# Kernel optimization log

Measured on AMD Instinct MI355X. Metric: run time of the kernel, lower is better.

Reference implementation:

```python
import jax, jax.numpy as jnp
import numpy as np

N = 100_000      # points
F = 64           # feature dim
B = 4            # graphs in batch
POOL_RAD = 0.2   # voxel size
D = 8            # static upper bound on voxels per spatial dim
M_MAX = 1024     # static upper bound on number of nonempty clusters


def setup_inputs() -> dict:
    key = jax.random.key(0)
    k1, k2, k3 = jax.random.split(key, 3)
    pos = jax.random.uniform(k1, (N, 3), dtype=jnp.float32)
    x = jax.random.normal(k2, (N, F), dtype=jnp.float32)
    batch = jnp.sort(jax.random.randint(k3, (N,), 0, B)).astype(jnp.int32)
    return {"pos": pos, "x": x, "batch": batch}


def reference(pos, x, batch):
    batch = batch.astype(jnp.int32)
    rad = jnp.asarray(POOL_RAD, pos.dtype)
    # --- voxel_grid clustering (start = min - rad/2 as in the torch module) ---
    start = pos.min(axis=0) - rad * 0.5
    coords = jnp.clip(jnp.floor((pos - start) / rad).astype(jnp.int32), 0, D - 1)  # [N,3]
    vox = ((batch * D + coords[:, 0]) * D + coords[:, 1]) * D + coords[:, 2]       # [N]
    V = B * D * D * D
    # --- consecutive_cluster + scatter mean of positions ---
    ones = jnp.ones((pos.shape[0],), pos.dtype)
    counts = jax.ops.segment_sum(ones, vox, num_segments=V)       # [V]
    sum_pos = jax.ops.segment_sum(pos, vox, num_segments=V)       # [V,3]
    nonempty = counts > 0
    # compact nonempty voxels to static M_MAX slots (padding duplicates voxel idx 0;
    # argmin tie-breaking to the first index keeps duplicates inert)
    idx = jnp.nonzero(nonempty, size=M_MAX, fill_value=0)[0]      # [M_MAX]
    valid = jnp.arange(M_MAX) < jnp.sum(nonempty)                 # [M_MAX]
    centroids = sum_pos[idx] / jnp.maximum(counts[idx], 1.0)[:, None]  # [M_MAX,3]
    new_batch = idx // (D * D * D)                                # [M_MAX]
    # --- nearest: assign each point to nearest cluster centroid in same graph ---
    d2 = (jnp.sum(pos * pos, axis=1)[:, None]
          - 2.0 * pos @ centroids.T
          + jnp.sum(centroids * centroids, axis=1)[None, :])      # [N, M_MAX]
    big = jnp.asarray(1e30, pos.dtype)
    d2 = jnp.where((batch[:, None] == new_batch[None, :]) & valid[None, :], d2, big)
    assign = jnp.argmin(d2, axis=1)                               # [N]
    # --- scatter max of features into clusters (empty clusters -> 0, as in PyG) ---
    x_pool = jax.ops.segment_max(x, assign, num_segments=M_MAX)   # [M_MAX, F]
    x_pool = jnp.where(jnp.isfinite(x_pool), x_pool, jnp.zeros_like(x_pool))
    return x_pool, centroids, new_batch, valid
```

## Files before the change

### kernel.cpp

```cpp
#include <hip/hip_runtime.h>
#include <stdint.h>

#define DGRID 8
#define NVOX  2048
#define NBATCH 4
#define MMAX  1024
#define FDIM  64
#define WIN   1024

__device__ __forceinline__ unsigned encf(float f){
  unsigned u = __float_as_uint(f);
  return (u & 0x80000000u) ? ~u : (u | 0x80000000u);
}
__device__ __forceinline__ float decf(unsigned e){
  unsigned u = (e & 0x80000000u) ? (e ^ 0x80000000u) : ~e;
  return __uint_as_float(u);
}


__global__ __launch_bounds__(256) void k_minpart(const float* __restrict__ pos,
    int N, unsigned* __restrict__ bmin, int* __restrict__ counts,
    int* __restrict__ clustCnt){
  if (blockIdx.x < 8) counts[blockIdx.x * 256 + threadIdx.x] = 0;
  else if (blockIdx.x < 12) clustCnt[(blockIdx.x - 8) * 256 + threadIdx.x] = 0;
  unsigned m0 = 0xFFFFFFFFu, m1 = 0xFFFFFFFFu, m2 = 0xFFFFFFFFu;
  int stride = gridDim.x * blockDim.x;
  for (int i = blockIdx.x * blockDim.x + threadIdx.x; i < N; i += stride){
    unsigned e0 = encf(pos[3*i+0]); if (e0 < m0) m0 = e0;
    unsigned e1 = encf(pos[3*i+1]); if (e1 < m1) m1 = e1;
    unsigned e2 = encf(pos[3*i+2]); if (e2 < m2) m2 = e2;
  }
  #pragma unroll
  for (int off = 32; off > 0; off >>= 1){
    unsigned t0 = __shfl_down(m0, off); if (t0 < m0) m0 = t0;
    unsigned t1 = __shfl_down(m1, off); if (t1 < m1) m1 = t1;
    unsigned t2 = __shfl_down(m2, off); if (t2 < m2) m2 = t2;
  }
  __shared__ unsigned sm[4][3];
  int wv = threadIdx.x >> 6, lane = threadIdx.x & 63;
  if (lane == 0){ sm[wv][0] = m0; sm[wv][1] = m1; sm[wv][2] = m2; }
  __syncthreads();
  if (threadIdx.x == 0){
    unsigned a0 = sm[0][0], a1 = sm[0][1], a2 = sm[0][2];
    for (int k = 1; k < 4; k++){
      if (sm[k][0] < a0) a0 = sm[k][0];
      if (sm[k][1] < a1) a1 = sm[k][1];
      if (sm[k][2] < a2) a2 = sm[k][2];
    }
    bmin[blockIdx.x*3+0] = a0;
    bmin[blockIdx.x*3+1] = a1;
    bmin[blockIdx.x*3+2] = a2;
  }
}

__global__ __launch_bounds__(256) void k_voxcnt(const float* __restrict__ pos,
    const int* __restrict__ batch, int N, const unsigned* __restrict__ bmin,
    int* __restrict__ vox, int* __restrict__ counts){
  __shared__ unsigned smin[3];
  if (threadIdx.x < 64){
    unsigned a0 = bmin[threadIdx.x*3+0];
    unsigned a1 = bmin[threadIdx.x*3+1];
    unsigned a2 = bmin[threadIdx.x*3+2];
    #pragma unroll
    for (int off = 32; off > 0; off >>= 1){
      unsigned t0 = __shfl_down(a0, off); if (t0 < a0) a0 = t0;
      unsigned t1 = __shfl_down(a1, off); if (t1 < a1) a1 = t1;
      unsigned t2 = __shfl_down(a2, off); if (t2 < a2) a2 = t2;
    }
    if (threadIdx.x == 0){ smin[0] = a0; smin[1] = a1; smin[2] = a2; }
  }
  __syncthreads();
  int i = blockIdx.x * 256 + threadIdx.x;
  if (i >= N) return;
  float s0 = __fsub_rn(decf(smin[0]), 0.1f);
  float s1 = __fsub_rn(decf(smin[1]), 0.1f);
  float s2 = __fsub_rn(decf(smin[2]), 0.1f);
  float q0 = __fdiv_rn(__fsub_rn(pos[3*i+0], s0), 0.2f);
  float q1 = __fdiv_rn(__fsub_rn(pos[3*i+1], s1), 0.2f);
  float q2 = __fdiv_rn(__fsub_rn(pos[3*i+2], s2), 0.2f);
  int c0 = (int)floorf(q0); c0 = c0 < 0 ? 0 : (c0 > DGRID-1 ? DGRID-1 : c0);
  int c1 = (int)floorf(q1); c1 = c1 < 0 ? 0 : (c1 > DGRID-1 ? DGRID-1 : c1);
  int c2 = (int)floorf(q2); c2 = c2 < 0 ? 0 : (c2 > DGRID-1 ? DGRID-1 : c2);
  int v = ((batch[i]*DGRID + c0)*DGRID + c1)*DGRID + c2;
  vox[i] = v;
  atomicAdd(&counts[v], 1);
}

__global__ __launch_bounds__(64) void k_scan_fast(const int* __restrict__ counts,
    int* Mout, int* batchStartC, int* batchPtr, int* __restrict__ idxOfCluster){
  int lane = threadIdx.x;
  int cs[32];
  int ne = 0, tot = 0;
  #pragma unroll
  for (int j = 0; j < 32; j++){
    int c = counts[lane*32 + j];
    cs[j] = c;
    ne += (c > 0) ? 1 : 0;
    tot += c;
  }
  int inc = ne, incT = tot;
  #pragma unroll
  for (int off = 1; off < 64; off <<= 1){
    int t  = __shfl_up(inc,  off);
    int tt = __shfl_up(incT, off);
    if (lane >= off){ inc += t; incT += tt; }
  }
  int exne = inc - ne;
  int exT  = incT - tot;
  int run = exne;
  #pragma unroll
  for (int j = 0; j < 32; j++){
    if (cs[j] > 0){
      if (run < MMAX) idxOfCluster[run] = lane*32 + j;
      run++;
    }
  }
  int M = __shfl(run, 63);
  for (int m = M + lane; m < MMAX; m += 64) idxOfCluster[m] = 0;
  int ex0  = __shfl(exne, 0),  ex16 = __shfl(exne, 16);
  int ex32 = __shfl(exne, 32), ex48 = __shfl(exne, 48);
  int t0 = __shfl(exT, 0),  t16 = __shfl(exT, 16);
  int t32 = __shfl(exT, 32), t48 = __shfl(exT, 48);
  int tN = __shfl(incT, 63);
  if (lane == 0){
    Mout[0] = M;
    batchStartC[0] = ex0;  batchStartC[1] = ex16;
    batchStartC[2] = ex32; batchStartC[3] = ex48;
    batchStartC[NBATCH] = (M < MMAX) ? M : MMAX;
    batchPtr[0] = t0;  batchPtr[1] = t16;
    batchPtr[2] = t32; batchPtr[3] = t48;
    batchPtr[4] = tN;
  }
}

__global__ __launch_bounds__(256) void k_wavesum2(const float* __restrict__ pos,
    const int* __restrict__ vox, const int* __restrict__ counts,
    const int* __restrict__ batchPtr, float4* __restrict__ centv){
  __shared__ int   svox[WIN];
  __shared__ float spos[WIN*3];
  int wave = threadIdx.x >> 6, lane = threadIdx.x & 63;
  int v = blockIdx.x * 4 + wave;
  int b = (blockIdx.x * 4) >> 9;
  int lo = batchPtr[b], hi = batchPtr[b+1];
  int cnt = counts[v];
  float sx = 0.f, sy = 0.f, sz = 0.f;
  for (int base = lo; base < hi; base += WIN){
    for (int t = threadIdx.x; t < WIN; t += 256){
      int i = base + t;
      int vv = (i < hi) ? vox[i] : -1;
      svox[t] = vv;
      if (vv >= 0){
        spos[3*t+0] = pos[3*i+0];
        spos[3*t+1] = pos[3*i+1];
        spos[3*t+2] = pos[3*i+2];
      }
    }
    __syncthreads();
    #pragma unroll 4
    for (int sub = 0; sub < WIN/64; sub++){
      unsigned long long mask = __ballot(svox[sub*64 + lane] == v);
      while (mask){
        int j = __ffsll(mask) - 1;
        mask &= mask - 1;
        int tt = sub*64 + j;
        sx = __fadd_rn(sx, spos[3*tt+0]);
        sy = __fadd_rn(sy, spos[3*tt+1]);
        sz = __fadd_rn(sz, spos[3*tt+2]);
      }
    }
    __syncthreads();
  }
  if (lane == 0){
    float den = fmaxf((float)cnt, 1.0f);
    float cx = __fdiv_rn(sx, den);
    float cy = __fdiv_rn(sy, den);
    float cz = __fdiv_rn(sz, den);
    float c2 = __fadd_rn(__fadd_rn(__fmul_rn(cx,cx), __fmul_rn(cy,cy)),
                         __fmul_rn(cz,cz));
    centv[v] = make_float4(cx, cy, cz, c2);
  }
}

__global__ __launch_bounds__(256) void k_argmin2(const float* __restrict__ pos,
    const int* __restrict__ batch, int N, const float4* __restrict__ centv,
    const int* __restrict__ idxOfCluster, const int* __restrict__ Mout,
    const int* __restrict__ batchStartC, int* __restrict__ assign,
    int* __restrict__ clustCnt, float* __restrict__ outC,
    float* __restrict__ outNB, float* __restrict__ outValid){
  __shared__ float4 sc[MMAX];
  __shared__ int h[MMAX];
  for (int m = threadIdx.x; m < MMAX; m += 256){
    sc[m] = centv[idxOfCluster[m]];
    h[m] = 0;
  }
  __syncthreads();
  if (blockIdx.x == 0){
    int M = Mout[0];
    for (int m = threadIdx.x; m < MMAX; m += 256){
      float4 cc = sc[m];
      outC[3*m+0] = cc.x; outC[3*m+1] = cc.y; outC[3*m+2] = cc.z;
      outNB[m] = (float)(idxOfCluster[m] >> 9);
      outValid[m] = (m < M) ? 1.0f : 0.0f;
    }
  }
  int i = blockIdx.x * 256 + threadIdx.x;
  if (i < N){
    float px = pos[3*i+0], py = pos[3*i+1], pz = pos[3*i+2];
    float p2 = __fadd_rn(__fadd_rn(__fmul_rn(px,px), __fmul_rn(py,py)), __fmul_rn(pz,pz));
    int b = batch[i];
    int mlo = batchStartC[b], mhi = batchStartC[b+1];
    float best = 3.402823466e+38f;
    int bm = mlo;
    for (int m = mlo; m < mhi; m++){
      float4 cc = sc[m];
      float dot = __fadd_rn(__fadd_rn(__fmul_rn(px,cc.x), __fmul_rn(py,cc.y)),
                            __fmul_rn(pz,cc.z));
      float d2  = __fadd_rn(__fsub_rn(p2, __fmul_rn(2.0f, dot)), cc.w);
      if (d2 < best){ best = d2; bm = m; }
    }
    assign[i] = bm;
    atomicAdd(&h[bm], 1);
  }
  __syncthreads();
  for (int t = threadIdx.x; t < MMAX; t += 256){
    int c = h[t];
    if (c > 0) atomicAdd(&clustCnt[t], c);
  }
}

__global__ __launch_bounds__(64) void k_cbase2(const int* __restrict__ clustCnt,
    int* __restrict__ clustBase, int* __restrict__ cur){
  int lane = threadIdx.x;
  int cs[16]; int tot = 0;
  #pragma unroll
  for (int j = 0; j < 16; j++){ cs[j] = clustCnt[lane*16 + j]; tot += cs[j]; }
  int inc = tot;
  #pragma unroll
  for (int off = 1; off < 64; off <<= 1){
    int t = __shfl_up(inc, off);
    if (lane >= off) inc += t;
  }
  int bb = inc - tot;
  #pragma unroll
  for (int j = 0; j < 16; j++){
    clustBase[lane*16 + j] = bb;
    cur[lane*16 + j] = bb;
    bb += cs[j];
  }
}

__global__ __launch_bounds__(256) void k_scatter2s(const int* __restrict__ assign,
    int N, int* __restrict__ cur, int* __restrict__ idx_sorted){
  int i = blockIdx.x * 256 + threadIdx.x;
  if (i >= N) return;
  int m = assign[i];
  int p = atomicAdd(&cur[m], 1);
  idx_sorted[p] = i;
}

__global__ __launch_bounds__(256) void k_xmax(const float* __restrict__ x,
    const int* __restrict__ idx_sorted, const int* __restrict__ clustBase,
    const int* __restrict__ clustCnt, float* __restrict__ outX){
  int w = blockIdx.x * 4 + (threadIdx.x >> 6);
  int lane = threadIdx.x & 63;
  if (w >= MMAX) return;
  int lo = clustBase[w], cnt = clustCnt[w];
  float mx = -3.402823466e+38f;
  int k = 0;
  for (; k + 4 <= cnt; k += 4){
    int r0 = idx_sorted[lo+k+0], r1 = idx_sorted[lo+k+1];
    int r2 = idx_sorted[lo+k+2], r3 = idx_sorted[lo+k+3];
    float a = x[(size_t)r0 * FDIM + lane];
    float b = x[(size_t)r1 * FDIM + lane];
    float c = x[(size_t)r2 * FDIM + lane];
    float d = x[(size_t)r3 * FDIM + lane];
    mx = fmaxf(mx, fmaxf(fmaxf(a, b), fmaxf(c, d)));
  }
  for (; k < cnt; k++){
    int r0 = idx_sorted[lo+k];
    mx = fmaxf(mx, x[(size_t)r0 * FDIM + lane]);
  }
  outX[w * FDIM + lane] = (cnt > 0) ? mx : 0.0f;
}


__global__ __launch_bounds__(256) void k_init(unsigned* startEnc, int* batchCnt){
  int t = threadIdx.x;
  if (t < 3) startEnc[t] = 0xFFFFFFFFu;
  if (t < NBATCH) batchCnt[t] = 0;
}

__global__ __launch_bounds__(256) void k_min_hist(const float* __restrict__ pos,
    const int* __restrict__ batch, int N, unsigned* startEnc, int* batchCnt){
  __shared__ int sbin[NBATCH];
  if (threadIdx.x < NBATCH) sbin[threadIdx.x] = 0;
  __syncthreads();
  unsigned m0 = 0xFFFFFFFFu, m1 = 0xFFFFFFFFu, m2 = 0xFFFFFFFFu;
  int stride = gridDim.x * blockDim.x;
  for (int i = blockIdx.x * blockDim.x + threadIdx.x; i < N; i += stride){
    unsigned e0 = encf(pos[3*i+0]); if (e0 < m0) m0 = e0;
    unsigned e1 = encf(pos[3*i+1]); if (e1 < m1) m1 = e1;
    unsigned e2 = encf(pos[3*i+2]); if (e2 < m2) m2 = e2;
    atomicAdd(&sbin[batch[i]], 1);
  }
  #pragma unroll
  for (int off = 32; off > 0; off >>= 1){
    unsigned t0 = __shfl_down(m0, off); if (t0 < m0) m0 = t0;
    unsigned t1 = __shfl_down(m1, off); if (t1 < m1) m1 = t1;
    unsigned t2 = __shfl_down(m2, off); if (t2 < m2) m2 = t2;
  }
  if ((threadIdx.x & 63) == 0){
    atomicMin(&startEnc[0], m0);
    atomicMin(&startEnc[1], m1);
    atomicMin(&startEnc[2], m2);
  }
  __syncthreads();
  if (threadIdx.x < NBATCH) atomicAdd(&batchCnt[threadIdx.x], sbin[threadIdx.x]);
}

__global__ __launch_bounds__(256) void k_vox(const float* __restrict__ pos,
    const int* __restrict__ batch, int N, const unsigned* __restrict__ startEnc,
    int* __restrict__ vox, int* __restrict__ counts){
  int i = blockIdx.x * blockDim.x + threadIdx.x;
  if (i >= N) return;
  float s0 = __fsub_rn(decf(startEnc[0]), 0.1f);
  float s1 = __fsub_rn(decf(startEnc[1]), 0.1f);
  float s2 = __fsub_rn(decf(startEnc[2]), 0.1f);
  float q0 = __fdiv_rn(__fsub_rn(pos[3*i+0], s0), 0.2f);
  float q1 = __fdiv_rn(__fsub_rn(pos[3*i+1], s1), 0.2f);
  float q2 = __fdiv_rn(__fsub_rn(pos[3*i+2], s2), 0.2f);
  int c0 = (int)floorf(q0); c0 = c0 < 0 ? 0 : (c0 > DGRID-1 ? DGRID-1 : c0);
  int c1 = (int)floorf(q1); c1 = c1 < 0 ? 0 : (c1 > DGRID-1 ? DGRID-1 : c1);
  int c2 = (int)floorf(q2); c2 = c2 < 0 ? 0 : (c2 > DGRID-1 ? DGRID-1 : c2);
  int v = ((batch[i]*DGRID + c0)*DGRID + c1)*DGRID + c2;
  vox[i] = v;
  atomicAdd(&counts[v], 1);
}

__global__ __launch_bounds__(64) void k_scan_old(const int* __restrict__ counts,
    const int* __restrict__ batchCnt, int* batchPtr, int* Mout,
    int* batchStartC, int* __restrict__ idxOfCluster, int* __restrict__ voxBase){
  int lane = threadIdx.x;
  int cs[32];
  int ne = 0, tot = 0;
  #pragma unroll
  for (int j = 0; j < 32; j++){
    int c = counts[lane*32 + j];
    cs[j] = c;
    ne += (c > 0) ? 1 : 0;
    tot += c;
  }
  int inc = ne, incT = tot;
  #pragma unroll
  for (int off = 1; off < 64; off <<= 1){
    int t  = __shfl_up(inc,  off);
    int tt = __shfl_up(incT, off);
    if (lane >= off){ inc += t; incT += tt; }
  }
  int exne = inc - ne;
  int bb   = incT - tot;
  int run = exne;
  #pragma unroll
  for (int j = 0; j < 32; j++){
    voxBase[lane*32 + j] = bb;
    bb += cs[j];
    if (cs[j] > 0){
      if (run < MMAX) idxOfCluster[run] = lane*32 + j;
      run++;
    }
  }
  int M = __shfl(run, 63);
  for (int m = M + lane; m < MMAX; m += 64) idxOfCluster[m] = 0;
  int ex0  = __shfl(exne, 0);
  int ex16 = __shfl(exne, 16);
  int ex32 = __shfl(exne, 32);
  int ex48 = __shfl(exne, 48);
  if (lane == 0){
    Mout[0] = M;
    int acc = 0;
    for (int b = 0; b < NBATCH; b++){ batchPtr[b] = acc; acc += batchCnt[b]; }
    batchPtr[NBATCH] = acc;
    batchStartC[0] = ex0;  batchStartC[1] = ex16;
    batchStartC[2] = ex32; batchStartC[3] = ex48;
    batchStartC[NBATCH] = (M < MMAX) ? M : MMAX;
  }
}

__global__ __launch_bounds__(64) void k_sum(const float* __restrict__ pos,
    const int* __restrict__ vox, const int* __restrict__ counts,
    const int* __restrict__ batchPtr, float* __restrict__ sum_pos){
  int v = blockIdx.x * 64 + threadIdx.x;
  if (v >= NVOX) return;
  int b = v >> 9;
  int lo = batchPtr[b], hi = batchPtr[b+1];
  float sx = 0.f, sy = 0.f, sz = 0.f;
  if (counts[v] > 0){
    for (int i = lo; i < hi; i++){
      if (vox[i] == v){
        sx = __fadd_rn(sx, pos[3*i+0]);
        sy = __fadd_rn(sy, pos[3*i+1]);
        sz = __fadd_rn(sz, pos[3*i+2]);
      }
    }
  }
  sum_pos[3*v+0] = sx;
  sum_pos[3*v+1] = sy;
  sum_pos[3*v+2] = sz;
}

__global__ __launch_bounds__(256) void k_cent(const float* __restrict__ sum_pos,
    const int* __restrict__ counts, const int* __restrict__ idxOfCluster,
    const int* __restrict__ Mout, float4* __restrict__ cent4,
    float* __restrict__ outC, float* __restrict__ outNB, float* __restrict__ outValid){
  int m = blockIdx.x * blockDim.x + threadIdx.x;
  if (m >= MMAX) return;
  int M = Mout[0];
  int v = idxOfCluster[m];
  float den = fmaxf((float)counts[v], 1.0f);
  float cx = __fdiv_rn(sum_pos[3*v+0], den);
  float cy = __fdiv_rn(sum_pos[3*v+1], den);
  float cz = __fdiv_rn(sum_pos[3*v+2], den);
  float c2 = __fadd_rn(__fadd_rn(__fmul_rn(cx,cx), __fmul_rn(cy,cy)), __fmul_rn(cz,cz));
  cent4[m] = make_float4(cx, cy, cz, c2);
  outC[3*m+0] = cx; outC[3*m+1] = cy; outC[3*m+2] = cz;
  outNB[m] = (float)(v >> 9);
  outValid[m] = (m < M) ? 1.0f : 0.0f;
}

__global__ __launch_bounds__(256) void k_assign_slow(const float* __restrict__ pos,
    const float* __restrict__ x, const int* __restrict__ batch, int N,
    const float4* __restrict__ cent4, const int* __restrict__ batchStartC,
    unsigned* __restrict__ encMax){
  __shared__ float4 sc[MMAX];
  for (int m = threadIdx.x; m < MMAX; m += blockDim.x) sc[m] = cent4[m];
  __syncthreads();
  int i = blockIdx.x * blockDim.x + threadIdx.x;
  if (i >= N) return;
  float px = pos[3*i+0], py = pos[3*i+1], pz = pos[3*i+2];
  float p2 = __fadd_rn(__fadd_rn(__fmul_rn(px,px), __fmul_rn(py,py)), __fmul_rn(pz,pz));
  int b = batch[i];
  int mlo = batchStartC[b], mhi = batchStartC[b+1];
  float best = 3.402823466e+38f;
  int bm = mlo;
  for (int m = mlo; m < mhi; m++){
    float4 c = sc[m];
    float dot = __fadd_rn(__fadd_rn(__fmul_rn(px,c.x), __fmul_rn(py,c.y)),
                          __fmul_rn(pz,c.z));
    float d2  = __fadd_rn(__fsub_rn(p2, __fmul_rn(2.0f, dot)), c.w);
    if (d2 < best){ best = d2; bm = m; }
  }
  unsigned* dst = encMax + bm * FDIM;
  const float4* xi = (const float4*)(x + (size_t)i * FDIM);
  #pragma unroll
  for (int f4 = 0; f4 < FDIM/4; f4++){
    float4 xv = xi[f4];
    atomicMax(&dst[4*f4+0], encf(xv.x));
    atomicMax(&dst[4*f4+1], encf(xv.y));
    atomicMax(&dst[4*f4+2], encf(xv.z));
    atomicMax(&dst[4*f4+3], encf(xv.w));
  }
}
__global__ __launch_bounds__(256) void k_decode(const unsigned* __restrict__ encMax,
    float* __restrict__ outX){
  int t = blockIdx.x * blockDim.x + threadIdx.x;
  if (t >= MMAX * FDIM) return;
  unsigned e = encMax[t];
  outX[t] = (e == 0u) ? 0.0f : decf(e);
}


extern "C" void kernel_launch(void* const* d_in, const int* in_sizes, int n_in,
                              void* d_out, int out_size, void* d_ws, size_t ws_size,
                              hipStream_t stream){
  const float* pos   = (const float*)d_in[0];
  const float* x     = (const float*)d_in[1];
  const int*   batch = (const int*)d_in[2];
  const int N = in_sizes[2];

  char* w = (char*)d_ws;
  unsigned* bmin         = (unsigned*)(w + 0);
  unsigned* startEnc     = (unsigned*)(w + 768);
  int*      batchCnt     = (int*)(w + 784);
  int*      batchPtr     = (int*)(w + 800);
  int*      Mout         = (int*)(w + 832);
  int*      batchStartC  = (int*)(w + 848);
  int*      counts       = (int*)(w + 896);
  int*      voxBase      = (int*)(w + 9088);
  float*    sum_pos      = (float*)(w + 17280);
  int*      idxOfCluster = (int*)(w + 41856);
  float4*   cent4        = (float4*)(w + 45952);
  int*      clustCnt     = (int*)(w + 62336);
  int*      clustBase    = (int*)(w + 66432);
  int*      cur          = (int*)(w + 70528);
  float4*   centv        = (float4*)(w + 74624);
  unsigned* encMax       = (unsigned*)(w + 107392);
  int*      vox          = (int*)(w + 369536);
  size_t aOff = 369536 + (size_t)N * 4;
  int*      assign       = (int*)(w + aOff);
  int*      idx_sorted   = (int*)(w + aOff) + N;
  size_t need = aOff + (size_t)N * 8;
  const bool fast = (ws_size >= need);

  float* outX     = (float*)d_out;
  float* outC     = outX + MMAX * FDIM;
  float* outNB    = outC + MMAX * 3;
  float* outValid = outNB + MMAX;

  const int nb = (N + 255) / 256;
  if (fast){
    k_minpart<<<64, 256, 0, stream>>>(pos, N, bmin, counts, clustCnt);
    k_voxcnt<<<nb, 256, 0, stream>>>(pos, batch, N, bmin, vox, counts);
    k_scan_fast<<<1, 64, 0, stream>>>(counts, Mout, batchStartC, batchPtr,
                                      idxOfCluster);
    k_wavesum2<<<NVOX / 4, 256, 0, stream>>>(pos, vox, counts, batchPtr, centv);
    k_argmin2<<<nb, 256, 0, stream>>>(pos, batch, N, centv, idxOfCluster, Mout,
                                      batchStartC, assign, clustCnt,
                                      outC, outNB, outValid);
    k_cbase2<<<1, 64, 0, stream>>>(clustCnt, clustBase, cur);
    k_scatter2s<<<nb, 256, 0, stream>>>(assign, N, cur, idx_sorted);
    k_xmax<<<MMAX / 4, 256, 0, stream>>>(x, idx_sorted, clustBase, clustCnt, outX);
  } else {
    k_init<<<1, 256, 0, stream>>>(startEnc, batchCnt);
    hipMemsetAsync(counts, 0, NVOX * 4, stream);
    hipMemsetAsync(encMax, 0, MMAX * FDIM * 4, stream);
    k_min_hist<<<256, 256, 0, stream>>>(pos, batch, N, startEnc, batchCnt);
    k_vox<<<nb, 256, 0, stream>>>(pos, batch, N, startEnc, vox, counts);
    k_scan_old<<<1, 64, 0, stream>>>(counts, batchCnt, batchPtr, Mout, batchStartC,
                                     idxOfCluster, voxBase);
    k_sum<<<(NVOX + 63) / 64, 64, 0, stream>>>(pos, vox, counts, batchPtr, sum_pos);
    k_cent<<<MMAX / 256, 256, 0, stream>>>(sum_pos, counts, idxOfCluster, Mout,
                                           cent4, outC, outNB, outValid);
    k_assign_slow<<<nb, 256, 0, stream>>>(pos, x, batch, N, cent4, batchStartC, encMax);
    k_decode<<<(MMAX * FDIM + 255) / 256, 256, 0, stream>>>(encMax, outX);
  }
}
```

Before: 172.5 us.

## Fuse the whole pipeline into one cooperative kernel with a counting sort by voxel

Replaces the chain of eight small kernel launches with a single cooperative kernel. Its phases (min reduction, voxel histogram, scans, centroids, argmin, cluster sort, feature max) are separated by grid-wide syncs. Centroid sums now come from per-chunk voxel histograms and a counting sort of positions into voxel order, instead of each wave scanning a window of points. This removes launch gaps and the window scan, but adds about eight grid barriers and a larger workspace requirement. It also deletes the old slow fallback kernels and keeps the previous multi-kernel path as the fallback if the cooperative launch fails.

```diff
diff --git a/kernel.cpp b/kernel.cpp
--- a/kernel.cpp
+++ b/kernel.cpp
@@ -1,12 +1,16 @@
 #include <hip/hip_runtime.h>
+#include <hip/hip_cooperative_groups.h>
 #include <stdint.h>
+
+namespace cg = cooperative_groups;
 
 #define DGRID 8
 #define NVOX  2048
 #define NBATCH 4
 #define MMAX  1024
 #define FDIM  64
-#define WIN   1024
+#define GRP   20
+#define MAXG  20
 
 __device__ __forceinline__ unsigned encf(float f){
   unsigned u = __float_as_uint(f);
@@ -15,6 +19,351 @@
 __device__ __forceinline__ float decf(unsigned e){
   unsigned u = (e & 0x80000000u) ? (e ^ 0x80000000u) : ~e;
   return __uint_as_float(u);
+}
+
+__global__ __launch_bounds__(256) void k_mega(
+    const float* __restrict__ pos, const float* __restrict__ x,
+    const int* __restrict__ batch, int N, int nchunks, int ngroups,
+    unsigned* __restrict__ bminP, unsigned* __restrict__ gminG,
+    int* __restrict__ Mout, int* __restrict__ batchStartC,
+    int* __restrict__ counts, int* __restrict__ voxBaseG,
+    int* __restrict__ idxOfCluster, int* __restrict__ clustCnt,
+    int* __restrict__ clustBaseG, int* __restrict__ clustRank,
+    float4* __restrict__ centv, int* __restrict__ gsum,
+    int* __restrict__ chunkHist, float* __restrict__ pos_sorted,
+    float* __restrict__ outX, float* __restrict__ outC,
+    float* __restrict__ outNB, float* __restrict__ outValid){
+  cg::grid_group grid = cg::this_grid();
+  __shared__ long long smemq[40960/8];
+  char* smem = (char*)smemq;
+  const int tid  = threadIdx.x;
+  const int blk  = blockIdx.x;
+  const int lane = tid & 63;
+  const int wv   = tid >> 6;
+  int* assign     = (int*)pos_sorted;
+  int* idx_sorted = assign + N;
+
+  {
+    if (blk < 8)       counts[blk*256 + tid] = 0;
+    else if (blk < 12) clustCnt[(blk-8)*256 + tid] = 0;
+    else if (blk < 16) clustRank[(blk-12)*256 + tid] = 0;
+    unsigned m0 = 0xFFFFFFFFu, m1 = 0xFFFFFFFFu, m2 = 0xFFFFFFFFu;
+    int stride = gridDim.x * 256;
+    for (int i = blk*256 + tid; i < N; i += stride){
+      unsigned e0 = encf(pos[3*i+0]); if (e0 < m0) m0 = e0;
+      unsigned e1 = encf(pos[3*i+1]); if (e1 < m1) m1 = e1;
+      unsigned e2 = encf(pos[3*i+2]); if (e2 < m2) m2 = e2;
+    }
+    #pragma unroll
+    for (int off = 32; off > 0; off >>= 1){
+      unsigned t0 = __shfl_down(m0, off); if (t0 < m0) m0 = t0;
+      unsigned t1 = __shfl_down(m1, off); if (t1 < m1) m1 = t1;
+      unsigned t2 = __shfl_down(m2, off); if (t2 < m2) m2 = t2;
+    }
+    unsigned* sm = (unsigned*)smem;
+    if (lane == 0){ sm[wv*3+0] = m0; sm[wv*3+1] = m1; sm[wv*3+2] = m2; }
+    __syncthreads();
+    if (tid == 0){
+      unsigned a0 = sm[0], a1 = sm[1], a2 = sm[2];
+      for (int k = 1; k < 4; k++){
+        if (sm[k*3+0] < a0) a0 = sm[k*3+0];
+        if (sm[k*3+1] < a1) a1 = sm[k*3+1];
+        if (sm[k*3+2] < a2) a2 = sm[k*3+2];
+      }
+      bminP[0*512 + blk] = a0;
+      bminP[1*512 + blk] = a1;
+      bminP[2*512 + blk] = a2;
+    }
+  }
+  grid.sync();
+
+  {
+    unsigned* smin = (unsigned*)smem;
+    int* hist = (int*)(smem + 256);
+    if (wv < 3){
+      unsigned a = 0xFFFFFFFFu;
+      for (int i = lane; i < (int)gridDim.x; i += 64){
+        unsigned t = bminP[wv*512 + i];
+        if (t < a) a = t;
+      }
+      #pragma unroll
+      for (int off = 32; off > 0; off >>= 1){
+        unsigned t = __shfl_down(a, off); if (t < a) a = t;
+      }
+      if (lane == 0) smin[wv] = a;
+    }
+    for (int t = tid; t < NVOX; t += 256) hist[t] = 0;
+    __syncthreads();
+    int c = blk;
+    if (c < nchunks){
+      int i = c*256 + tid;
+      if (i < N){
+        float s0 = __fsub_rn(decf(smin[0]), 0.1f);
+        float s1 = __fsub_rn(decf(smin[1]), 0.1f);
+        float s2 = __fsub_rn(decf(smin[2]), 0.1f);
+        float q0 = __fdiv_rn(__fsub_rn(pos[3*i+0], s0), 0.2f);
+        float q1 = __fdiv_rn(__fsub_rn(pos[3*i+1], s1), 0.2f);
+        float q2 = __fdiv_rn(__fsub_rn(pos[3*i+2], s2), 0.2f);
+        int c0 = (int)floorf(q0); c0 = c0 < 0 ? 0 : (c0 > DGRID-1 ? DGRID-1 : c0);
+        int c1 = (int)floorf(q1); c1 = c1 < 0 ? 0 : (c1 > DGRID-1 ? DGRID-1 : c1);
+        int c2 = (int)floorf(q2); c2 = c2 < 0 ? 0 : (c2 > DGRID-1 ? DGRID-1 : c2);
+        int v = ((batch[i]*DGRID + c0)*DGRID + c1)*DGRID + c2;
+        atomicAdd(&hist[v], 1);
+      }
+    }
+    __syncthreads();
+    if (c < nchunks)
+      for (int t = tid; t < NVOX; t += 256) chunkHist[c*NVOX + t] = hist[t];
+    if (blk == 0 && tid < 3) gminG[tid] = smin[tid];
+  }
+  grid.sync();
+
+  if (blk < ngroups*8){
+    int g = blk >> 3;
+    int v = (blk & 7)*256 + tid;
+    int c0 = g*GRP, c1 = min(nchunks, c0 + GRP);
+    int s = 0;
+    for (int c = c0; c < c1; c++) s += chunkHist[c*NVOX + v];
+    gsum[g*NVOX + v] = s;
+  }
+  grid.sync();
+
+  if (blk < 8){
+    int v = blk*256 + tid;
+    int run = 0;
+    for (int g = 0; g < ngroups; g++){
+      int t = gsum[g*NVOX + v];
+      gsum[g*NVOX + v] = run;
+      run += t;
+    }
+    counts[v] = run;
+  }
+  grid.sync();
+
+  {
+    int* sBase  = (int*)smem;
+    int* rowCnt = (int*)(smem + 8192);
+    if (wv == 0){
+      int cs[32];
+      int ne = 0, tot = 0;
+      #pragma unroll
+      for (int j = 0; j < 32; j++){
+        int c2 = counts[lane*32 + j];
+        cs[j] = c2; ne += (c2 > 0) ? 1 : 0; tot += c2;
+      }
+      int inc = ne, incT = tot;
+      #pragma unroll
+      for (int off = 1; off < 64; off <<= 1){
+        int t  = __shfl_up(inc,  off);
+        int tt = __shfl_up(incT, off);
+        if (lane >= off){ inc += t; incT += tt; }
+      }
+      int exne = inc - ne, exT = incT - tot;
+      int run = exne, bb = exT;
+      #pragma unroll
+      for (int j = 0; j < 32; j++){
+        sBase[lane*32 + j] = bb;
+        if (blk == 0) voxBaseG[lane*32 + j] = bb;
+        bb += cs[j];
+        if (cs[j] > 0){
+          if (blk == 0 && run < MMAX) idxOfCluster[run] = lane*32 + j;
+          run++;
+        }
+      }
+      int M = __shfl(run, 63);
+      int ex0  = __shfl(exne, 0),  ex16 = __shfl(exne, 16);
+      int ex32 = __shfl(exne, 32), ex48 = __shfl(exne, 48);
+      if (blk == 0){
+        for (int m = M + lane; m < MMAX; m += 64) idxOfCluster[m] = 0;
+        if (lane == 0){
+          Mout[0] = M;
+          batchStartC[0] = ex0;  batchStartC[1] = ex16;
+          batchStartC[2] = ex32; batchStartC[3] = ex48;
+          batchStartC[NBATCH] = (M < MMAX) ? M : MMAX;
+        }
+      }
+    } else {
+      for (int t = tid - 64; t < 4*NVOX; t += 192) rowCnt[t] = 0;
+    }
+    __syncthreads();
+    int c = blk;
+    bool haveChunk = (c < nchunks);
+    if (haveChunk){
+      int g = c / GRP, cg0 = g*GRP;
+      for (int t = tid; t < NVOX; t += 256){
+        int b = sBase[t] + gsum[g*NVOX + t];
+        for (int cc = cg0; cc < c; cc++) b += chunkHist[cc*NVOX + t];
+        sBase[t] = b;
+      }
+    }
+    __syncthreads();
+    int v = -1, rank = 0;
+    float px = 0.f, py = 0.f, pz = 0.f;
+    bool valid = false;
+    if (haveChunk){
+      int i = c*256 + tid;
+      valid = (i < N);
+      if (valid){
+        px = pos[3*i+0]; py = pos[3*i+1]; pz = pos[3*i+2];
+        float s0 = __fsub_rn(decf(gminG[0]), 0.1f);
+        float s1 = __fsub_rn(decf(gminG[1]), 0.1f);
+        float s2 = __fsub_rn(decf(gminG[2]), 0.1f);
+        float q0 = __fdiv_rn(__fsub_rn(px, s0), 0.2f);
+        float q1 = __fdiv_rn(__fsub_rn(py, s1), 0.2f);
+        float q2 = __fdiv_rn(__fsub_rn(pz, s2), 0.2f);
+        int c0 = (int)floorf(q0); c0 = c0 < 0 ? 0 : (c0 > DGRID-1 ? DGRID-1 : c0);
+        int c1 = (int)floorf(q1); c1 = c1 < 0 ? 0 : (c1 > DGRID-1 ? DGRID-1 : c1);
+        int c2 = (int)floorf(q2); c2 = c2 < 0 ? 0 : (c2 > DGRID-1 ? DGRID-1 : c2);
+        v = ((batch[c*256 + tid]*DGRID + c0)*DGRID + c1)*DGRID + c2;
+      }
+      int cnt = 0;
+      #pragma unroll 8
+      for (int j = 0; j < 64; j++){
+        int vj = __shfl(v, j);
+        if (vj == v){
+          cnt++;
+          if (j < lane) rank++;
+        }
+      }
+      if (valid && rank == 0) rowCnt[wv*NVOX + v] = cnt;
+    }
+    __syncthreads();
+    if (valid){
+      int pre = 0;
+      for (int rr = 0; rr < wv; rr++) pre += rowCnt[rr*NVOX + v];
+      int dst = sBase[v] + pre + rank;
+      pos_sorted[3*dst+0] = px;
+      pos_sorted[3*dst+1] = py;
+      pos_sorted[3*dst+2] = pz;
+    }
+  }
+  grid.sync();
+
+  if (blk < 32 && tid < 64){
+    int v = blk*64 + tid;
+    int lo = voxBaseG[v], cnt = counts[v];
+    const float* p = pos_sorted + 3*(size_t)lo;
+    float sx = 0.f, sy = 0.f, sz = 0.f;
+    int k = 0;
+    for (; k + 4 <= cnt; k += 4){
+      float a0 = p[0],  a1 = p[1],  a2 = p[2];
+      float b0 = p[3],  b1 = p[4],  b2 = p[5];
+      float c0 = p[6],  c1 = p[7],  c2 = p[8];
+      float d0 = p[9],  d1 = p[10], d2 = p[11];
+      sx = __fadd_rn(__fadd_rn(__fadd_rn(__fadd_rn(sx, a0), b0), c0), d0);
+      sy = __fadd_rn(__fadd_rn(__fadd_rn(__fadd_rn(sy, a1), b1), c1), d1);
+      sz = __fadd_rn(__fadd_rn(__fadd_rn(__fadd_rn(sz, a2), b2), c2), d2);
+      p += 12;
+    }
+    for (; k < cnt; k++){
+      sx = __fadd_rn(sx, p[0]);
+      sy = __fadd_rn(sy, p[1]);
+      sz = __fadd_rn(sz, p[2]);
+      p += 3;
+    }
+    float den = fmaxf((float)cnt, 1.0f);
+    float cx = __fdiv_rn(sx, den);
+    float cy = __fdiv_rn(sy, den);
+    float cz = __fdiv_rn(sz, den);
+    float c2 = __fadd_rn(__fadd_rn(__fmul_rn(cx,cx), __fmul_rn(cy,cy)),
+                         __fmul_rn(cz,cz));
+    centv[v] = make_float4(cx, cy, cz, c2);
+  }
+  grid.sync();
+
+  {
+    float4* sc = (float4*)smem;
+    int* h = (int*)(smem + 16384);
+    for (int m = tid; m < MMAX; m += 256){
+      sc[m] = centv[idxOfCluster[m]];
+      h[m] = 0;
+    }
+    __syncthreads();
+    if (blk == 0){
+      int M = Mout[0];
+      for (int m = tid; m < MMAX; m += 256){
+        float4 cc = sc[m];
+        outC[3*m+0] = cc.x; outC[3*m+1] = cc.y; outC[3*m+2] = cc.z;
+        outNB[m] = (float)(idxOfCluster[m] >> 9);
+        outValid[m] = (m < M) ? 1.0f : 0.0f;
+      }
+    }
+    int i = blk*256 + tid;
+    if (i < N){
+      float px = pos[3*i+0], py = pos[3*i+1], pz = pos[3*i+2];
+      float p2 = __fadd_rn(__fadd_rn(__fmul_rn(px,px), __fmul_rn(py,py)), __fmul_rn(pz,pz));
+      int b = batch[i];
+      int mlo = batchStartC[b], mhi = batchStartC[b+1];
+      float best = 3.402823466e+38f;
+      int bm = mlo;
+      for (int m = mlo; m < mhi; m++){
+        float4 cc = sc[m];
+        float dot = __fadd_rn(__fadd_rn(__fmul_rn(px,cc.x), __fmul_rn(py,cc.y)),
+                              __fmul_rn(pz,cc.z));
+        float d2  = __fadd_rn(__fsub_rn(p2, __fmul_rn(2.0f, dot)), cc.w);
+        if (d2 < best){ best = d2; bm = m; }
+      }
+      assign[i] = bm;
+      atomicAdd(&h[bm], 1);
+    }
+    __syncthreads();
+    for (int t = tid; t < MMAX; t += 256){
+      int cc = h[t];
+      if (cc > 0) atomicAdd(&clustCnt[t], cc);
+    }
+  }
+  grid.sync();
+
+  {
+    int* cb = (int*)smem;
+    if (wv == 0){
+      int cs[16]; int tot = 0;
+      #pragma unroll
+      for (int j = 0; j < 16; j++){ cs[j] = clustCnt[lane*16 + j]; tot += cs[j]; }
+      int inc = tot;
+      #pragma unroll
+      for (int off = 1; off < 64; off <<= 1){
+        int t = __shfl_up(inc, off);
+        if (lane >= off) inc += t;
+      }
+      int bb = inc - tot;
+      #pragma unroll
+      for (int j = 0; j < 16; j++){
+        cb[lane*16 + j] = bb;
+        if (blk == 0) clustBaseG[lane*16 + j] = bb;
+        bb += cs[j];
+      }
+    }
+    __syncthreads();
+    int i = blk*256 + tid;
+    if (i < N){
+      int m = assign[i];
+      int r = atomicAdd(&clustRank[m], 1);
+      idx_sorted[cb[m] + r] = i;
+    }
+  }
+  grid.sync();
+
+  if (blk < 256){
+    int w2 = blk*4 + wv;
+    int lo = clustBaseG[w2], cnt = clustCnt[w2];
+    float mx = -3.402823466e+38f;
+    int k = 0;
+    for (; k + 4 <= cnt; k += 4){
+      int r0 = idx_sorted[lo+k+0], r1 = idx_sorted[lo+k+1];
+      int r2 = idx_sorted[lo+k+2], r3 = idx_sorted[lo+k+3];
+      float a = x[(size_t)r0 * FDIM + lane];
+      float b = x[(size_t)r1 * FDIM + lane];
+      float c = x[(size_t)r2 * FDIM + lane];
+      float d = x[(size_t)r3 * FDIM + lane];
+      mx = fmaxf(mx, fmaxf(fmaxf(a, b), fmaxf(c, d)));
+    }
+    for (; k < cnt; k++){
+      int r0 = idx_sorted[lo+k];
+      mx = fmaxf(mx, x[(size_t)r0 * FDIM + lane]);
+    }
+    outX[w2*FDIM + lane] = (cnt > 0) ? mx : 0.0f;
+  }
 }
 
 
@@ -133,6 +482,7 @@
   }
 }
 
+#define WIN 1024
 __global__ __launch_bounds__(256) void k_wavesum2(const float* __restrict__ pos,
     const int* __restrict__ vox, const int* __restrict__ counts,
     const int* __restrict__ batchPtr, float4* __restrict__ centv){
@@ -284,253 +634,75 @@
 }
 
 
-__global__ __launch_bounds__(256) void k_init(unsigned* startEnc, int* batchCnt){
-  int t = threadIdx.x;
-  if (t < 3) startEnc[t] = 0xFFFFFFFFu;
-  if (t < NBATCH) batchCnt[t] = 0;
-}
-
-__global__ __launch_bounds__(256) void k_min_hist(const float* __restrict__ pos,
-    const int* __restrict__ batch, int N, unsigned* startEnc, int* batchCnt){
-  __shared__ int sbin[NBATCH];
-  if (threadIdx.x < NBATCH) sbin[threadIdx.x] = 0;
-  __syncthreads();
-  unsigned m0 = 0xFFFFFFFFu, m1 = 0xFFFFFFFFu, m2 = 0xFFFFFFFFu;
-  int stride = gridDim.x * blockDim.x;
-  for (int i = blockIdx.x * blockDim.x + threadIdx.x; i < N; i += stride){
-    unsigned e0 = encf(pos[3*i+0]); if (e0 < m0) m0 = e0;
-    unsigned e1 = encf(pos[3*i+1]); if (e1 < m1) m1 = e1;
-    unsigned e2 = encf(pos[3*i+2]); if (e2 < m2) m2 = e2;
-    atomicAdd(&sbin[batch[i]], 1);
-  }
-  #pragma unroll
-  for (int off = 32; off > 0; off >>= 1){
-    unsigned t0 = __shfl_down(m0, off); if (t0 < m0) m0 = t0;
-    unsigned t1 = __shfl_down(m1, off); if (t1 < m1) m1 = t1;
-    unsigned t2 = __shfl_down(m2, off); if (t2 < m2) m2 = t2;
-  }
-  if ((threadIdx.x & 63) == 0){
-    atomicMin(&startEnc[0], m0);
-    atomicMin(&startEnc[1], m1);
-    atomicMin(&startEnc[2], m2);
-  }
-  __syncthreads();
-  if (threadIdx.x < NBATCH) atomicAdd(&batchCnt[threadIdx.x], sbin[threadIdx.x]);
-}
-
-__global__ __launch_bounds__(256) void k_vox(const float* __restrict__ pos,
-    const int* __restrict__ batch, int N, const unsigned* __restrict__ startEnc,
-    int* __restrict__ vox, int* __restrict__ counts){
-  int i = blockIdx.x * blockDim.x + threadIdx.x;
-  if (i >= N) return;
-  float s0 = __fsub_rn(decf(startEnc[0]), 0.1f);
-  float s1 = __fsub_rn(decf(startEnc[1]), 0.1f);
-  float s2 = __fsub_rn(decf(startEnc[2]), 0.1f);
-  float q0 = __fdiv_rn(__fsub_rn(pos[3*i+0], s0), 0.2f);
-  float q1 = __fdiv_rn(__fsub_rn(pos[3*i+1], s1), 0.2f);
-  float q2 = __fdiv_rn(__fsub_rn(pos[3*i+2], s2), 0.2f);
-  int c0 = (int)floorf(q0); c0 = c0 < 0 ? 0 : (c0 > DGRID-1 ? DGRID-1 : c0);
-  int c1 = (int)floorf(q1); c1 = c1 < 0 ? 0 : (c1 > DGRID-1 ? DGRID-1 : c1);
-  int c2 = (int)floorf(q2); c2 = c2 < 0 ? 0 : (c2 > DGRID-1 ? DGRID-1 : c2);
-  int v = ((batch[i]*DGRID + c0)*DGRID + c1)*DGRID + c2;
-  vox[i] = v;
-  atomicAdd(&counts[v], 1);
-}
-
-__global__ __launch_bounds__(64) void k_scan_old(const int* __restrict__ counts,
-    const int* __restrict__ batchCnt, int* batchPtr, int* Mout,
-    int* batchStartC, int* __restrict__ idxOfCluster, int* __restrict__ voxBase){
-  int lane = threadIdx.x;
-  int cs[32];
-  int ne = 0, tot = 0;
-  #pragma unroll
-  for (int j = 0; j < 32; j++){
-    int c = counts[lane*32 + j];
-    cs[j] = c;
-    ne += (c > 0) ? 1 : 0;
-    tot += c;
-  }
-  int inc = ne, incT = tot;
-  #pragma unroll
-  for (int off = 1; off < 64; off <<= 1){
-    int t  = __shfl_up(inc,  off);
-    int tt = __shfl_up(incT, off);
-    if (lane >= off){ inc += t; incT += tt; }
-  }
-  int exne = inc - ne;
-  int bb   = incT - tot;
-  int run = exne;
-  #pragma unroll
-  for (int j = 0; j < 32; j++){
-    voxBase[lane*32 + j] = bb;
-    bb += cs[j];
-    if (cs[j] > 0){
-      if (run < MMAX) idxOfCluster[run] = lane*32 + j;
-      run++;
-    }
-  }
-  int M = __shfl(run, 63);
-  for (int m = M + lane; m < MMAX; m += 64) idxOfCluster[m] = 0;
-  int ex0  = __shfl(exne, 0);
-  int ex16 = __shfl(exne, 16);
-  int ex32 = __shfl(exne, 32);
-  int ex48 = __shfl(exne, 48);
-  if (lane == 0){
-    Mout[0] = M;
-    int acc = 0;
-    for (int b = 0; b < NBATCH; b++){ batchPtr[b] = acc; acc += batchCnt[b]; }
-    batchPtr[NBATCH] = acc;
-    batchStartC[0] = ex0;  batchStartC[1] = ex16;
-    batchStartC[2] = ex32; batchStartC[3] = ex48;
-    batchStartC[NBATCH] = (M < MMAX) ? M : MMAX;
-  }
-}
-
-__global__ __launch_bounds__(64) void k_sum(const float* __restrict__ pos,
-    const int* __restrict__ vox, const int* __restrict__ counts,
-    const int* __restrict__ batchPtr, float* __restrict__ sum_pos){
-  int v = blockIdx.x * 64 + threadIdx.x;
-  if (v >= NVOX) return;
-  int b = v >> 9;
-  int lo = batchPtr[b], hi = batchPtr[b+1];
-  float sx = 0.f, sy = 0.f, sz = 0.f;
-  if (counts[v] > 0){
-    for (int i = lo; i < hi; i++){
-      if (vox[i] == v){
-        sx = __fadd_rn(sx, pos[3*i+0]);
-        sy = __fadd_rn(sy, pos[3*i+1]);
-        sz = __fadd_rn(sz, pos[3*i+2]);
-      }
-    }
-  }
-  sum_pos[3*v+0] = sx;
-  sum_pos[3*v+1] = sy;
-  sum_pos[3*v+2] = sz;
-}
-
-__global__ __launch_bounds__(256) void k_cent(const float* __restrict__ sum_pos,
-    const int* __restrict__ counts, const int* __restrict__ idxOfCluster,
-    const int* __restrict__ Mout, float4* __restrict__ cent4,
-    float* __restrict__ outC, float* __restrict__ outNB, float* __restrict__ outValid){
-  int m = blockIdx.x * blockDim.x + threadIdx.x;
-  if (m >= MMAX) return;
-  int M = Mout[0];
-  int v = idxOfCluster[m];
-  float den = fmaxf((float)counts[v], 1.0f);
-  float cx = __fdiv_rn(sum_pos[3*v+0], den);
-  float cy = __fdiv_rn(sum_pos[3*v+1], den);
-  float cz = __fdiv_rn(sum_pos[3*v+2], den);
-  float c2 = __fadd_rn(__fadd_rn(__fmul_rn(cx,cx), __fmul_rn(cy,cy)), __fmul_rn(cz,cz));
-  cent4[m] = make_float4(cx, cy, cz, c2);
-  outC[3*m+0] = cx; outC[3*m+1] = cy; outC[3*m+2] = cz;
-  outNB[m] = (float)(v >> 9);
-  outValid[m] = (m < M) ? 1.0f : 0.0f;
-}
-
-__global__ __launch_bounds__(256) void k_assign_slow(const float* __restrict__ pos,
-    const float* __restrict__ x, const int* __restrict__ batch, int N,
-    const float4* __restrict__ cent4, const int* __restrict__ batchStartC,
-    unsigned* __restrict__ encMax){
-  __shared__ float4 sc[MMAX];
-  for (int m = threadIdx.x; m < MMAX; m += blockDim.x) sc[m] = cent4[m];
-  __syncthreads();
-  int i = blockIdx.x * blockDim.x + threadIdx.x;
-  if (i >= N) return;
-  float px = pos[3*i+0], py = pos[3*i+1], pz = pos[3*i+2];
-  float p2 = __fadd_rn(__fadd_rn(__fmul_rn(px,px), __fmul_rn(py,py)), __fmul_rn(pz,pz));
-  int b = batch[i];
-  int mlo = batchStartC[b], mhi = batchStartC[b+1];
-  float best = 3.402823466e+38f;
-  int bm = mlo;
-  for (int m = mlo; m < mhi; m++){
-    float4 c = sc[m];
-    float dot = __fadd_rn(__fadd_rn(__fmul_rn(px,c.x), __fmul_rn(py,c.y)),
-                          __fmul_rn(pz,c.z));
-    float d2  = __fadd_rn(__fsub_rn(p2, __fmul_rn(2.0f, dot)), c.w);
-    if (d2 < best){ best = d2; bm = m; }
-  }
-  unsigned* dst = encMax + bm * FDIM;
-  const float4* xi = (const float4*)(x + (size_t)i * FDIM);
-  #pragma unroll
-  for (int f4 = 0; f4 < FDIM/4; f4++){
-    float4 xv = xi[f4];
-    atomicMax(&dst[4*f4+0], encf(xv.x));
-    atomicMax(&dst[4*f4+1], encf(xv.y));
-    atomicMax(&dst[4*f4+2], encf(xv.z));
-    atomicMax(&dst[4*f4+3], encf(xv.w));
-  }
-}
-__global__ __launch_bounds__(256) void k_decode(const unsigned* __restrict__ encMax,
-    float* __restrict__ outX){
-  int t = blockIdx.x * blockDim.x + threadIdx.x;
-  if (t >= MMAX * FDIM) return;
-  unsigned e = encMax[t];
-  outX[t] = (e == 0u) ? 0.0f : decf(e);
-}
-
-
 extern "C" void kernel_launch(void* const* d_in, const int* in_sizes, int n_in,
                               void* d_out, int out_size, void* d_ws, size_t ws_size,
                               hipStream_t stream){
   const float* pos   = (const float*)d_in[0];
   const float* x     = (const float*)d_in[1];
   const int*   batch = (const int*)d_in[2];
-  const int N = in_sizes[2];
+  int N = in_sizes[2];
 
   char* w = (char*)d_ws;
-  unsigned* bmin         = (unsigned*)(w + 0);
-  unsigned* startEnc     = (unsigned*)(w + 768);
-  int*      batchCnt     = (int*)(w + 784);
-  int*      batchPtr     = (int*)(w + 800);
-  int*      Mout         = (int*)(w + 832);
-  int*      batchStartC  = (int*)(w + 848);
-  int*      counts       = (int*)(w + 896);
-  int*      voxBase      = (int*)(w + 9088);
-  float*    sum_pos      = (float*)(w + 17280);
-  int*      idxOfCluster = (int*)(w + 41856);
-  float4*   cent4        = (float4*)(w + 45952);
-  int*      clustCnt     = (int*)(w + 62336);
-  int*      clustBase    = (int*)(w + 66432);
-  int*      cur          = (int*)(w + 70528);
-  float4*   centv        = (float4*)(w + 74624);
-  unsigned* encMax       = (unsigned*)(w + 107392);
-  int*      vox          = (int*)(w + 369536);
-  size_t aOff = 369536 + (size_t)N * 4;
-  int*      assign       = (int*)(w + aOff);
-  int*      idx_sorted   = (int*)(w + aOff) + N;
-  size_t need = aOff + (size_t)N * 8;
-  const bool fast = (ws_size >= need);
+  unsigned* bminP        = (unsigned*)(w + 0);
+  unsigned* gminG        = (unsigned*)(w + 6144);
+  int*      Mout         = (int*)(w + 6208);
+  int*      batchStartC  = (int*)(w + 6224);
+  int*      batchPtr     = (int*)(w + 6244);
+  int*      counts       = (int*)(w + 6272);
+  int*      voxBaseG     = (int*)(w + 14464);
+  int*      idxOfCluster = (int*)(w + 22656);
+  int*      clustCnt     = (int*)(w + 26752);
+  int*      clustBaseG   = (int*)(w + 30848);
+  int*      clustRank    = (int*)(w + 34944);
+  float4*   centv        = (float4*)(w + 39040);
+  int*      gsum         = (int*)(w + 71808);
+  int*      chunkHist    = (int*)(w + 235648);
+
+  int nchunks = (N + 255) / 256;
+  int ngroups = (nchunks + GRP - 1) / GRP;
+  size_t psOff = 235648 + (size_t)nchunks * NVOX * 4;
+  float* pos_sorted = (float*)(w + psOff);
+  size_t needM = psOff + (size_t)N * 12;
 
   float* outX     = (float*)d_out;
   float* outC     = outX + MMAX * FDIM;
   float* outNB    = outC + MMAX * 3;
   float* outValid = outNB + MMAX;
 
+  int gridM = nchunks > 256 ? nchunks : 256;
+  bool mega_ok = (ws_size >= needM) && (ngroups <= MAXG) && (gridM <= 1024) && (N > 0);
+
+  if (mega_ok){
+    const float* pos_a = pos; const float* x_a = x; const int* batch_a = batch;
+    int N_a = N, nch_a = nchunks, ng_a = ngroups;
+    void* kargs[] = {
+      (void*)&pos_a, (void*)&x_a, (void*)&batch_a,
+      (void*)&N_a, (void*)&nch_a, (void*)&ng_a,
+      (void*)&bminP, (void*)&gminG, (void*)&Mout, (void*)&batchStartC,
+      (void*)&counts, (void*)&voxBaseG, (void*)&idxOfCluster, (void*)&clustCnt,
+      (void*)&clustBaseG, (void*)&clustRank, (void*)&centv, (void*)&gsum,
+      (void*)&chunkHist, (void*)&pos_sorted,
+      (void*)&outX, (void*)&outC, (void*)&outNB, (void*)&outValid
+    };
+    hipError_t e = hipLaunchCooperativeKernel((void*)k_mega, dim3(gridM), dim3(256),
+                                              kargs, 0, stream);
+    if (e == hipSuccess) return;
+    (void)hipGetLastError();
+  }
+
+  int*   vox        = chunkHist;
+  int*   assign     = (int*)pos_sorted;
+  int*   idx_sorted = assign + N;
+  int*   cur        = clustRank;
   const int nb = (N + 255) / 256;
-  if (fast){
-    k_minpart<<<64, 256, 0, stream>>>(pos, N, bmin, counts, clustCnt);
-    k_voxcnt<<<nb, 256, 0, stream>>>(pos, batch, N, bmin, vox, counts);
-    k_scan_fast<<<1, 64, 0, stream>>>(counts, Mout, batchStartC, batchPtr,
-                                      idxOfCluster);
-    k_wavesum2<<<NVOX / 4, 256, 0, stream>>>(pos, vox, counts, batchPtr, centv);
-    k_argmin2<<<nb, 256, 0, stream>>>(pos, batch, N, centv, idxOfCluster, Mout,
-                                      batchStartC, assign, clustCnt,
-                                      outC, outNB, outValid);
-    k_cbase2<<<1, 64, 0, stream>>>(clustCnt, clustBase, cur);
-    k_scatter2s<<<nb, 256, 0, stream>>>(assign, N, cur, idx_sorted);
-    k_xmax<<<MMAX / 4, 256, 0, stream>>>(x, idx_sorted, clustBase, clustCnt, outX);
-  } else {
-    k_init<<<1, 256, 0, stream>>>(startEnc, batchCnt);
-    hipMemsetAsync(counts, 0, NVOX * 4, stream);
-    hipMemsetAsync(encMax, 0, MMAX * FDIM * 4, stream);
-    k_min_hist<<<256, 256, 0, stream>>>(pos, batch, N, startEnc, batchCnt);
-    k_vox<<<nb, 256, 0, stream>>>(pos, batch, N, startEnc, vox, counts);
-    k_scan_old<<<1, 64, 0, stream>>>(counts, batchCnt, batchPtr, Mout, batchStartC,
-                                     idxOfCluster, voxBase);
-    k_sum<<<(NVOX + 63) / 64, 64, 0, stream>>>(pos, vox, counts, batchPtr, sum_pos);
-    k_cent<<<MMAX / 256, 256, 0, stream>>>(sum_pos, counts, idxOfCluster, Mout,
-                                           cent4, outC, outNB, outValid);
-    k_assign_slow<<<nb, 256, 0, stream>>>(pos, x, batch, N, cent4, batchStartC, encMax);
-    k_decode<<<(MMAX * FDIM + 255) / 256, 256, 0, stream>>>(encMax, outX);
-  }
-}
+  k_minpart<<<64, 256, 0, stream>>>(pos, N, bminP, counts, clustCnt);
+  k_voxcnt<<<nb, 256, 0, stream>>>(pos, batch, N, bminP, vox, counts);
+  k_scan_fast<<<1, 64, 0, stream>>>(counts, Mout, batchStartC, batchPtr, idxOfCluster);
+  k_wavesum2<<<NVOX / 4, 256, 0, stream>>>(pos, vox, counts, batchPtr, centv);
+  k_argmin2<<<nb, 256, 0, stream>>>(pos, batch, N, centv, idxOfCluster, Mout,
+                                    batchStartC, assign, clustCnt,
+                                    outC, outNB, outValid);
+  k_cbase2<<<1, 64, 0, stream>>>(clustCnt, clustBaseG, cur);
+  k_scatter2s<<<nb, 256, 0, stream>>>(assign, N, cur, idx_sorted);
+  k_xmax<<<MMAX / 4, 256, 0, stream>>>(x, idx_sorted, clustBaseG, clustCnt, outX);
+}
```

Result: slower. 473.8 us (+174.7%).
